# Performance work log

Measured on AMD Instinct MI355X. Metric: run time of the kernel, lower is better.

The kernel has to match this reference:

```python
import jax, jax.numpy as jnp
import numpy as np

B, L, D_MODEL = 8, 1024, 512
D_STATE, D_CONV, EXPAND = 16, 4, 2
D_INNER = EXPAND * D_MODEL          # 1024
DT_RANK = (D_MODEL + 15) // 16      # 32
D_FF = 4 * D_MODEL                  # 2048
EPS = 1e-12


def setup_inputs() -> dict:
    key = jax.random.key(0)
    ks = jax.random.split(key, 16)
    s = 0.02
    n = lambda k, shp: jax.random.normal(k, shp, dtype=jnp.float32) * s
    A = jnp.tile(jnp.arange(1, D_STATE + 1, dtype=jnp.float32)[None, :], (D_INNER, 1))
    return {
        "x": jax.random.normal(ks[0], (B, L, D_MODEL), dtype=jnp.float32),
        "in_proj_w": n(ks[1], (2 * D_INNER, D_MODEL)),
        "conv_w": n(ks[2], (D_INNER, 1, D_CONV)),
        "conv_b": jnp.zeros((D_INNER,), jnp.float32),
        "x_proj_w": n(ks[3], (DT_RANK + 2 * D_STATE, D_INNER)),
        "dt_proj_w": n(ks[4], (D_INNER, DT_RANK)),
        "dt_proj_b": jnp.full((D_INNER,), -4.0, jnp.float32),  # softplus(~-4) -> small dt
        "A_log": jnp.log(A),
        "D": jnp.ones((D_INNER,), jnp.float32),
        "out_proj_w": n(ks[5], (D_MODEL, D_INNER)),
        "ln1_g": jnp.ones((D_MODEL,), jnp.float32),
        "ln1_b": jnp.zeros((D_MODEL,), jnp.float32),
        "fc1_w": n(ks[6], (D_FF, D_MODEL)),
        "fc1_b": jnp.zeros((D_FF,), jnp.float32),
        "fc2_w": n(ks[7], (D_MODEL, D_FF)),
        "fc2_b": jnp.zeros((D_MODEL,), jnp.float32),
        "ln2_g": jnp.ones((D_MODEL,), jnp.float32),
        "ln2_b": jnp.zeros((D_MODEL,), jnp.float32),
    }


def _layernorm(x, g, b):
    m = jnp.mean(x, axis=-1, keepdims=True)
    v = jnp.var(x, axis=-1, keepdims=True)
    return (x - m) * jax.lax.rsqrt(v + EPS) * g + b


def _mamba(x, in_proj_w, conv_w, conv_b, x_proj_w, dt_proj_w, dt_proj_b, A_log, D, out_proj_w):
    # in_proj: [B,L,d_model] -> [B,L,2*d_inner]
    xz = jnp.einsum("bld,ed->ble", x, in_proj_w)
    u, z = jnp.split(xz, 2, axis=-1)                      # each [B,L,d_inner]
    # depthwise causal conv over time
    uc = jax.lax.conv_general_dilated(
        jnp.transpose(u, (0, 2, 1)), conv_w,
        window_strides=(1,), padding=[(D_CONV - 1, 0)],
        feature_group_count=D_INNER,
        dimension_numbers=("NCH", "OIH", "NCH"))
    u = jnp.transpose(uc, (0, 2, 1)) + conv_b             # [B,L,d_inner]
    u = jax.nn.silu(u)
    # x_proj -> dt, B, C
    x_dbl = jnp.einsum("bld,ed->ble", u, x_proj_w)
    dt, Bm, Cm = jnp.split(x_dbl, [DT_RANK, DT_RANK + D_STATE], axis=-1)
    dt = jax.nn.softplus(jnp.einsum("blr,dr->bld", dt, dt_proj_w) + dt_proj_b)  # [B,L,d_inner]
    A = -jnp.exp(A_log)                                   # [d_inner, d_state]
    deltaA = jnp.exp(dt[..., None] * A)                   # [B,L,d_inner,d_state]
    deltaBu = dt[..., None] * Bm[:, :, None, :] * u[..., None]

    def step(h, inp):
        dA_t, dBu_t, C_t = inp                            # [B,di,ds],[B,di,ds],[B,ds]
        h = h * dA_t + dBu_t
        y = jnp.einsum("bds,bs->bd", h, C_t)
        return h, y

    h0 = jnp.zeros((x.shape[0], D_INNER, D_STATE), x.dtype)
    _, ys = jax.lax.scan(step, h0, (jnp.transpose(deltaA, (1, 0, 2, 3)),
                                    jnp.transpose(deltaBu, (1, 0, 2, 3)),
                                    jnp.transpose(Cm, (1, 0, 2))))
    y = jnp.transpose(ys, (1, 0, 2)) + u * D              # [B,L,d_inner]
    y = y * jax.nn.silu(z)
    return jnp.einsum("ble,de->bld", y, out_proj_w)


def reference(x, in_proj_w, conv_w, conv_b, x_proj_w, dt_proj_w, dt_proj_b, A_log, D,
              out_proj_w, ln1_g, ln1_b, fc1_w, fc1_b, fc2_w, fc2_b, ln2_g, ln2_b):
    h = _mamba(x, in_proj_w, conv_w, conv_b, x_proj_w, dt_proj_w, dt_proj_b,
               A_log, D, out_proj_w)
    h = _layernorm(h + x, ln1_g, ln1_b)                   # dropout = identity (eval)
    # FeedForward with residual + LayerNorm
    f = jax.nn.gelu(jnp.einsum("bld,fd->blf", h, fc1_w) + fc1_b, approximate=False)
    f = jnp.einsum("blf,df->bld", f, fc2_w) + fc2_b
    return _layernorm(f + h, ln2_g, ln2_b)
```

## Files before the change

kernel.cpp:

```cpp
#include <hip/hip_runtime.h>
#include <hip/hip_bf16.h>
#include <math.h>

typedef __hip_bfloat16 bf16;
typedef unsigned short u16;
typedef unsigned int u32;
typedef __attribute__((ext_vector_type(8))) short short8;
typedef __attribute__((ext_vector_type(4))) float f32x4;
typedef __attribute__((ext_vector_type(4))) u32 u32x4;

#define B_  8
#define L_  1024
#define DM  512
#define DI  1024
#define DS  16
#define DR  32
#define DF  2048
#define M_  (B_ * L_)

__device__ __forceinline__ float b2f(bf16 x) { return __bfloat162float(x); }
__device__ __forceinline__ bf16  f2b(float x) { return __float2bfloat16(x); }
__device__ __forceinline__ u16   bu(bf16 x)  { return __builtin_bit_cast(u16, x); }
__device__ __forceinline__ float s2f(short x) { return b2f(__builtin_bit_cast(bf16, (u16)x)); }
__device__ __forceinline__ float uphi(u32 w) { return __builtin_bit_cast(float, w & 0xffff0000u); }
__device__ __forceinline__ float uplo(u32 w) { return __builtin_bit_cast(float, w << 16); }

__device__ __forceinline__ bool is_b16(const void* flag) {
    return ((const u16*)flag)[0] == 0x3F80;
}
__device__ __forceinline__ float ldr(const void* p, size_t i, bool b16) {
    return b16 ? b2f(((const bf16*)p)[i]) : ((const float*)p)[i];
}

__device__ __forceinline__ float fexp2(float x) {
#if __has_builtin(__builtin_amdgcn_exp2f)
    return __builtin_amdgcn_exp2f(x);
#else
    return __expf(x * 0.6931471805599453f);
#endif
}

__device__ __forceinline__ float fsoftplus(float v) {
    return (v > 20.f) ? v : __logf(1.f + __expf(v));
}

__device__ __forceinline__ float fgelu(float v) {
    const float x = v * 0.7071067811865475f;
    const float ax = fabsf(x);
    const float t = __builtin_amdgcn_rcpf(fmaf(0.3275911f, ax, 1.f));
    float p = fmaf(1.061405429f, t, -1.453152027f);
    p = fmaf(p, t, 1.421413741f);
    p = fmaf(p, t, -0.284496736f);
    p = fmaf(p, t, 0.254829592f);
    const float e = __expf(-ax * ax);
    float erf = 1.f - p * t * e;
    erf = (x < 0.f) ? -erf : erf;
    return 0.5f * v * (1.f + erf);
}

__device__ __forceinline__ void gload16(const bf16* g, bf16* l) {
    __builtin_amdgcn_global_load_lds(
        (const __attribute__((address_space(1))) unsigned int*)g,
        (__attribute__((address_space(3))) unsigned int*)l, 16, 0, 0);
}

__device__ __forceinline__ float fsilu(float x) {
    return x * __builtin_amdgcn_rcpf(1.f + __expf(-x));
}

#define CN0 (M_ * DM)
#define CN1 (CN0 + 2 * DI * DM)
#define CN2 (CN1 + 64 * DI)
#define CN3 (CN2 + DI * DR)
#define CN4 (CN3 + DM * DI)
#define CN5 (CN4 + DF * DM)
#define CN6 (CN5 + DM * DF)
#define CN7 (CN6 + DI * 4)
#define CN8 (CN7 + DI)
#define CN9 (CN8 + DI)
__global__ __launch_bounds__(256) void cvt_all_kernel(
    const void* s0, const void* s1, const void* s2, const void* s3,
    const void* s4, const void* s5, const void* s6, const void* s7,
    const void* s8, const void* s9,
    bf16* __restrict__ dst, const void* __restrict__ flag)
{
    const bool b16 = is_b16(flag);
    const long i = ((long)blockIdx.x * 256 + threadIdx.x) * 8;
    if (i >= CN9) return;
    const void* src; long off;
    if      (i < CN0) { src = s0; off = i; }
    else if (i < CN1) { src = s1; off = i - CN0; }
    else if (i < CN2) { src = s2; off = i - CN1; }
    else if (i < CN3) { src = s3; off = i - CN2; }
    else if (i < CN4) { src = s4; off = i - CN3; }
    else if (i < CN5) { src = s5; off = i - CN4; }
    else if (i < CN6) { src = s6; off = i - CN5; }
    else if (i < CN7) { src = s7; off = i - CN6; }
    else if (i < CN8) { src = s8; off = i - CN7; }
    else              { src = s9; off = i - CN8; }
    if (b16) {
        *(short8*)(dst + i) = *(const short8*)((const bf16*)src + off);
    } else {
        const float* f = (const float*)src + off;
        const f32x4 a = *(const f32x4*)f;
        const f32x4 b = *(const f32x4*)(f + 4);
        short8 o;
#pragma unroll
        for (int k = 0; k < 4; ++k) {
            o[k]     = (short)bu(f2b(a[k]));
            o[k + 4] = (short)bu(f2b(b[k]));
        }
        *(short8*)(dst + i) = o;
    }
}

template <int BM, int BN, int NT, int ACT, int PACK>
__global__ __launch_bounds__(NT) void mfma_gemm(
    const bf16* __restrict__ A, int lda,
    const bf16* __restrict__ W, int ldw,
    const void* __restrict__ bias,
    bf16* __restrict__ C, int ldc,
    int K, const void* __restrict__ flag,
    void* __restrict__ pk, void* __restrict__ pk2,
    const bf16* __restrict__ uin)
{
    constexpr int WN = (BN >= 128) ? 2 : 1;
    constexpr int CA = BM * 4 / NT;
    constexpr int CB = BN * 4 / NT;
    constexpr int BUF = (BM + BN) * 32;
    __shared__ __align__(16) bf16 smem[2 * BUF];
    const int tid  = threadIdx.x;
    const int wave = tid >> 6, lane = tid & 63;
    const int quad = lane >> 4, l16 = lane & 15;
    const u32 gx  = gridDim.x;
    const u32 nwg = gx * gridDim.y;
    const u32 lid = blockIdx.y * gx + blockIdx.x;
    const u32 swz = (lid & 7) * (nwg >> 3) + (lid >> 3);
    const int bm = (int)(swz / gx) * BM, bn = (int)(swz % gx) * BN;
    const int wm = (wave / WN) * 64, wn = (wave % WN) * 64;

    f32x4 acc[4][4];
#pragma unroll
    for (int i = 0; i < 4; ++i)
#pragma unroll
        for (int j = 0; j < 4; ++j) acc[i][j] = (f32x4){0.f, 0.f, 0.f, 0.f};

    auto load_tile = [&](int k0, int p) {
        bf16* As = smem + p * BUF;
        bf16* Ws = As + BM * 32;
#pragma unroll
        for (int j = 0; j < CA; ++j) {
            const int e = j * NT + tid;
            gload16(A + (size_t)(bm + (e >> 2)) * lda + k0 + (e & 3) * 8, As + e * 8);
        }
#pragma unroll
        for (int j = 0; j < CB; ++j) {
            const int e = j * NT + tid;
            gload16(W + (size_t)(bn + (e >> 2)) * ldw + k0 + (e & 3) * 8, Ws + e * 8);
        }
    };

    const int NIT = K >> 5;
    load_tile(0, 0);
    for (int it = 0; it < NIT; ++it) {
        __syncthreads();
        if (it + 1 < NIT) load_tile((it + 1) << 5, (it + 1) & 1);
        const bf16* As = smem + (it & 1) * BUF;
        const bf16* Ws = As + BM * 32;
        short8 af[4], wf[4];
#pragma unroll
        for (int mt = 0; mt < 4; ++mt)
            af[mt] = *(const short8*)(As + (wm + mt * 16 + l16) * 32 + quad * 8);
#pragma unroll
        for (int nt = 0; nt < 4; ++nt)
            wf[nt] = *(const short8*)(Ws + (wn + nt * 16 + l16) * 32 + quad * 8);
#pragma unroll
        for (int mt = 0; mt < 4; ++mt)
#pragma unroll
            for (int nt = 0; nt < 4; ++nt)
                acc[mt][nt] = __builtin_amdgcn_mfma_f32_16x16x32_bf16(
                    af[mt], wf[nt], acc[mt][nt], 0, 0, 0);
    }

    const bool b16 = bias ? is_b16(flag) : false;
#pragma unroll
    for (int nt = 0; nt < 4; ++nt) {
        const int col = bn + wn + nt * 16 + l16;
        const float bv = bias ? ldr(bias, col, b16) : 0.f;
#pragma unroll
        for (int mt = 0; mt < 4; ++mt)
#pragma unroll
            for (int i = 0; i < 4; ++i) {
                const int row = bm + wm + mt * 16 + quad * 4 + i;
                float v = acc[mt][nt][i] + bv;
                if (ACT == 1) v = fsoftplus(v);
                else if (ACT == 2) v = fgelu(v);
                if (PACK == 1) {
                    const float uv = b2f(uin[(size_t)row * ldc + col]);
                    ((float*)pk)[(size_t)row * ldc + col]  = v;
                    ((float*)pk2)[(size_t)row * ldc + col] = v * uv;
                } else {
                    C[(size_t)row * ldc + col] = f2b(v);
                }
            }
    }
    if (PACK == 2) {
#pragma unroll
        for (int mt = 0; mt < 4; ++mt)
#pragma unroll
            for (int i = 0; i < 4; ++i) {
                const int row = bm + wm + mt * 16 + quad * 4 + i;
                ((float*)pk)[(size_t)row * 16 + l16]  = acc[mt][2][i];
                ((float*)pk2)[(size_t)row * 16 + l16] = acc[mt][3][i];
            }
    }
}

__global__ __launch_bounds__(256) void conv_silu_kernel(
    const bf16* __restrict__ xz,
    const bf16* __restrict__ cw,
    const bf16* __restrict__ cb,
    const bf16* __restrict__ Dw,
    bf16* __restrict__ u,
    u32* __restrict__ ug)
{
    const int t  = blockIdx.x * 256 + threadIdx.x;
    const long t8 = (long)t * 8;
    const int d8  = (int)(t8 & (DI - 1));
    const int row = (int)(t8 >> 10);
    const int l   = row & (L_ - 1);

    short8 wraw[4];
#pragma unroll
    for (int k = 0; k < 4; ++k)
        wraw[k] = *(const short8*)(cw + (size_t)d8 * 4 + k * 8);
    const short8 cbv = *(const short8*)(cb + d8);
    const short8 dv  = *(const short8*)(Dw + d8);

    float acc[8];
#pragma unroll
    for (int i = 0; i < 8; ++i) acc[i] = s2f(cbv[i]);
#pragma unroll
    for (int j = 0; j < 4; ++j) {
        const int ls = l - 3 + j;
        if (ls >= 0) {
            const short8 xv = *(const short8*)(xz + (size_t)(row - 3 + j) * (2 * DI) + d8);
#pragma unroll
            for (int i = 0; i < 8; ++i) {
                const int f = i * 4 + j;
                acc[i] += s2f(wraw[f >> 3][f & 7]) * s2f(xv[i]);
            }
        }
    }
    const short8 zv = *(const short8*)(xz + (size_t)row * (2 * DI) + DI + d8);
    short8 us;
    u32x4 g0, g1;
#pragma unroll
    for (int i = 0; i < 8; ++i) {
        const float uv = fsilu(acc[i]);
        us[i] = (short)bu(f2b(uv));
        const float gz = fsilu(s2f(zv[i]));
        const float g2 = uv * s2f(dv[i]) * gz;
        const u32 p = ((u32)bu(f2b(g2)) << 16) | bu(f2b(gz));
        if (i < 4) g0[i] = p; else g1[i - 4] = p;
    }
    *(short8*)(u + t8) = us;
    *(u32x4*)(ug + t8) = g0;
    *(u32x4*)(ug + t8 + 4) = g1;
}

__global__ __launch_bounds__(256) void scan_kernel(
    const float* __restrict__ dtf,
    const float* __restrict__ duf,
    const float* __restrict__ Bf,
    const float* __restrict__ Cf,
    const u32* __restrict__ ug,
    const void* __restrict__ A_log,
    bf16* __restrict__ y,
    const void* __restrict__ flag)
{
    const bool b16 = is_b16(flag);
    const int tid = threadIdx.x;
    const int lane = tid & 63;
    const int s  = lane & 15;
    const int dl = tid >> 4;
    const int b = blockIdx.x >> 6, dch = blockIdx.x & 63;
    const int d0 = dch * 16, d = d0 + dl;
    const float AcL = -__expf(ldr(A_log, (size_t)d * DS + s, b16))
                      * 1.4426950408889634f;

    __shared__ __align__(16) float dt_s[16][68];
    __shared__ __align__(16) float du_s[16][68];
    __shared__ __align__(16) float B_s[16][68];
    __shared__ __align__(16) float C_s[16][68];
    __shared__ u32 ug_s[16][68];
    __shared__ bf16 y_s[16][72];
    __shared__ float p_s[16][16][33];

    const int c16 = tid & 15, r16 = tid >> 4;
    float rdt[4], rdu[4], rB[4], rC[4];
    u32 rug[4];
    const size_t base = (size_t)b * L_;

    auto load_chunk = [&](int l0) {
#pragma unroll
        for (int j = 0; j < 4; ++j) {
            const size_t row = base + l0 + r16 + 16 * j;
            rdt[j] = dtf[row * DI + d0 + c16];
            rdu[j] = duf[row * DI + d0 + c16];
            rug[j] = ug[row * DI + d0 + c16];
            rB[j]  = Bf[row * 16 + c16];
            rC[j]  = Cf[row * 16 + c16];
        }
    };
    auto store_chunk = [&]() {
#pragma unroll
        for (int j = 0; j < 4; ++j) {
            dt_s[c16][r16 + 16 * j] = rdt[j];
            du_s[c16][r16 + 16 * j] = rdu[j];
            ug_s[c16][r16 + 16 * j] = rug[j];
            B_s[c16][r16 + 16 * j]  = rB[j];
            C_s[c16][r16 + 16 * j]  = rC[j];
        }
    };

    float h = 0.f;
    float* const prow = &p_s[dl][s][0];
    load_chunk(0);
    for (int c = 0; c < 16; ++c) {
        store_chunk();
        __syncthreads();
        if (c < 15) load_chunk((c + 1) * 64);
#pragma unroll
        for (int g = 0; g < 2; ++g) {
#pragma unroll
            for (int w2 = 0; w2 < 2; ++w2) {
                const int w = g * 2 + w2;
                f32x4 dtw[4], duw[4], bw[4], cw[4];
#pragma unroll
                for (int q = 0; q < 4; ++q) {
                    dtw[q] = *(const f32x4*)&dt_s[dl][w * 16 + q * 4];
                    duw[q] = *(const f32x4*)&du_s[dl][w * 16 + q * 4];
                    bw[q]  = *(const f32x4*)&B_s[s][w * 16 + q * 4];
                    cw[q]  = *(const f32x4*)&C_s[s][w * 16 + q * 4];
                }
#pragma unroll
                for (int t = 0; t < 16; ++t) {
                    const float e = fexp2(dtw[t >> 2][t & 3] * AcL);
                    h = fmaf(h, e, duw[t >> 2][t & 3] * bw[t >> 2][t & 3]);
                    prow[w2 * 16 + t] = h * cw[t >> 2][t & 3];
                }
            }
            asm volatile("s_waitcnt lgkmcnt(0)" ::: "memory");
#pragma unroll
            for (int w2 = 0; w2 < 2; ++w2) {
                const int w = g * 2 + w2;
                const u32 ugw = ug_s[dl][w * 16 + s];
                float pr[16];
#pragma unroll
                for (int k = 0; k < 16; ++k) pr[k] = p_s[dl][k][w2 * 16 + s];
#pragma unroll
                for (int o = 8; o >= 1; o >>= 1)
#pragma unroll
                    for (int i = 0; i < o; ++i) pr[i] += pr[i + o];
                y_s[dl][w * 16 + s] = f2b(fmaf(pr[0], uplo(ugw), uphi(ugw)));
            }
        }
        __syncthreads();
#pragma unroll
        for (int j = 0; j < 4; ++j) {
            const size_t row = base + c * 64 + r16 + 16 * j;
            y[row * DI + d0 + c16] = y_s[c16][r16 + 16 * j];
        }
    }
}

template <int RMODE, int OMODE>
__global__ __launch_bounds__(256) void ln_kernel(
    const bf16* __restrict__ inp,
    const bf16* __restrict__ res,
    const void* __restrict__ g,
    const void* __restrict__ bb,
    void* __restrict__ out,
    const void* __restrict__ flag)
{
    const bool b16 = is_b16(flag);
    const int wv = threadIdx.x >> 6, lane = threadIdx.x & 63;
    const int row = blockIdx.x * 4 + wv;
    const size_t off = (size_t)row * DM;
    const int e = lane * 8;

    float v[8];
    const short8 iv = *(const short8*)(inp + off + e);
    const short8 rv = *(const short8*)(res + off + e);
#pragma unroll
    for (int i = 0; i < 8; ++i) v[i] = s2f(iv[i]) + s2f(rv[i]);

    float sum = 0.f, sq = 0.f;
#pragma unroll
    for (int i = 0; i < 8; ++i) { sum += v[i]; sq += v[i] * v[i]; }
#pragma unroll
    for (int o = 32; o >= 1; o >>= 1) {
        sum += __shfl_xor(sum, o);
        sq  += __shfl_xor(sq, o);
    }
    const float m = sum * (1.f / DM);
    const float var = sq * (1.f / DM) - m * m;
    const float inv = rsqrtf(fmaxf(var, 0.f) + 1e-12f);

    float gv[8], bv[8];
    if (b16) {
        const short8 gg = *(const short8*)((const bf16*)g + e);
        const short8 bg = *(const short8*)((const bf16*)bb + e);
#pragma unroll
        for (int i = 0; i < 8; ++i) { gv[i] = s2f(gg[i]); bv[i] = s2f(bg[i]); }
    } else {
        const float* gf = (const float*)g + e;
        const float* bf = (const float*)bb + e;
        const f32x4 g0 = *(const f32x4*)gf, g1 = *(const f32x4*)(gf + 4);
        const f32x4 b0 = *(const f32x4*)bf, b1 = *(const f32x4*)(bf + 4);
#pragma unroll
        for (int i = 0; i < 8; ++i) {
            gv[i] = i < 4 ? g0[i] : g1[i - 4];
            bv[i] = i < 4 ? b0[i] : b1[i - 4];
        }
    }
    float o[8];
#pragma unroll
    for (int i = 0; i < 8; ++i) o[i] = (v[i] - m) * inv * gv[i] + bv[i];

    if (OMODE == 2 && !b16) {
        f32x4 o0, o1;
#pragma unroll
        for (int i = 0; i < 4; ++i) { o0[i] = o[i]; o1[i] = o[i + 4]; }
        *(f32x4*)((float*)out + off + e) = o0;
        *(f32x4*)((float*)out + off + e + 4) = o1;
    } else {
        short8 os;
#pragma unroll
        for (int i = 0; i < 8; ++i) os[i] = (short)bu(f2b(o[i]));
        *(short8*)((bf16*)out + off + e) = os;
    }
}

extern "C" void kernel_launch(void* const* d_in, const int* in_sizes, int n_in,
                              void* d_out, int out_size, void* d_ws, size_t ws_size,
                              hipStream_t stream)
{
    (void)in_sizes; (void)n_in; (void)out_size; (void)ws_size;
    const void* x       = d_in[0];
    const void* in_w    = d_in[1];
    const void* conv_w  = d_in[2];
    const void* conv_b  = d_in[3];
    const void* xproj_w = d_in[4];
    const void* dt_w    = d_in[5];
    const void* dt_b    = d_in[6];
    const void* A_log   = d_in[7];
    const void* Dw      = d_in[8];
    const void* out_w   = d_in[9];
    const void* ln1_g   = d_in[10];
    const void* ln1_b   = d_in[11];
    const void* fc1_w   = d_in[12];
    const void* fc1_b   = d_in[13];
    const void* fc2_w   = d_in[14];
    const void* fc2_b   = d_in[15];
    const void* ln2_g   = d_in[16];
    const void* ln2_b   = d_in[17];
    const void* flag    = ln1_g;

    bf16* xb    = (bf16*)d_ws;
    bf16* inwb  = xb    + (size_t)M_ * DM;
    bf16* xpwb  = inwb  + (size_t)2 * DI * DM;
    bf16* dtwb  = xpwb  + (size_t)64 * DI;
    bf16* outwb = dtwb  + (size_t)DI * DR;
    bf16* fc1wb = outwb + (size_t)DM * DI;
    bf16* fc2wb = fc1wb + (size_t)DF * DM;
    bf16* cwb   = fc2wb + (size_t)DM * DF;
    bf16* cbb   = cwb   + (size_t)DI * 4;
    bf16* dwb   = cbb   + (size_t)DI;
    bf16* xz    = dwb   + (size_t)DI;
    bf16* u     = xz    + (size_t)M_ * 2 * DI;
    bf16* xdbl  = u     + (size_t)M_ * DI;
    float* dtf  = (float*)(xdbl + (size_t)M_ * 64);
    u32*  ugp   = (u32*)(dtf + (size_t)M_ * DI);
    float* Bfp  = (float*)(ugp + (size_t)M_ * DI);
    bf16* yb    = (bf16*)(Bfp + (size_t)M_ * 16);
    bf16* hb    = yb    + (size_t)M_ * DI;
    float* duf  = (float*)xz;
    float* Cfp  = (float*)hb;
    bf16* mo    = (bf16*)dtf;
    bf16* fb    = xz;
    bf16* f2b_  = yb;

    dim3 blk(256);
    cvt_all_kernel<<<dim3((CN9 / 8 + 255) / 256), blk, 0, stream>>>(
        x, in_w, xproj_w, dt_w, out_w, fc1_w, fc2_w, conv_w, conv_b, Dw,
        xb, flag);

    mfma_gemm<128, 128, 256, 0, 0><<<dim3(16, 64), blk, 0, stream>>>(
        xb, DM, inwb, DM, nullptr, xz, 2 * DI, DM, flag, nullptr, nullptr, nullptr);
    conv_silu_kernel<<<dim3(M_ * DI / 8 / 256), blk, 0, stream>>>(
        xz, cwb, cbb, dwb, u, ugp);
    mfma_gemm<128, 64, 128, 0, 2><<<dim3(1, 64), dim3(128), 0, stream>>>(
        u, DI, xpwb, DI, nullptr, xdbl, 64, DI, flag, Bfp, Cfp, nullptr);
    mfma_gemm<128, 128, 256, 1, 1><<<dim3(8, 64), blk, 0, stream>>>(
        xdbl, 64, dtwb, DR, dt_b, nullptr, DI, DR, flag, dtf, duf, u);
    scan_kernel<<<dim3(B_ * 64), blk, 0, stream>>>(
        dtf, duf, Bfp, Cfp, ugp, A_log, yb, flag);
    mfma_gemm<128, 128, 256, 0, 0><<<dim3(4, 64), blk, 0, stream>>>(
        yb, DI, outwb, DI, nullptr, mo, DM, DI, flag, nullptr, nullptr, nullptr);
    ln_kernel<1, 1><<<dim3(M_ / 4), blk, 0, stream>>>(
        mo, xb, ln1_g, ln1_b, hb, flag);
    mfma_gemm<128, 128, 256, 2, 0><<<dim3(16, 64), blk, 0, stream>>>(
        hb, DM, fc1wb, DM, fc1_b, fb, DF, DM, flag, nullptr, nullptr, nullptr);
    mfma_gemm<128, 128, 256, 0, 0><<<dim3(4, 64), blk, 0, stream>>>(
        fb, DF, fc2wb, DF, fc2_b, f2b_, DM, DF, flag, nullptr, nullptr, nullptr);
    ln_kernel<1, 2><<<dim3(M_ / 4), blk, 0, stream>>>(
        f2b_, hb, ln2_g, ln2_b, d_out, flag);
}
```

Measured before the change: 344.4 us.

## Fuse dt_proj GEMM and softplus into scan kernel via per-chunk MFMA

```diff
diff --git a/kernel.cpp b/kernel.cpp
--- a/kernel.cpp
+++ b/kernel.cpp
@@ -195,13 +195,7 @@
                 float v = acc[mt][nt][i] + bv;
                 if (ACT == 1) v = fsoftplus(v);
                 else if (ACT == 2) v = fgelu(v);
-                if (PACK == 1) {
-                    const float uv = b2f(uin[(size_t)row * ldc + col]);
-                    ((float*)pk)[(size_t)row * ldc + col]  = v;
-                    ((float*)pk2)[(size_t)row * ldc + col] = v * uv;
-                } else {
-                    C[(size_t)row * ldc + col] = f2b(v);
-                }
+                C[(size_t)row * ldc + col] = f2b(v);
             }
     }
     if (PACK == 2) {
@@ -270,12 +264,14 @@
 }
 
 __global__ __launch_bounds__(256) void scan_kernel(
-    const float* __restrict__ dtf,
-    const float* __restrict__ duf,
+    const bf16* __restrict__ xdbl,
+    const bf16* __restrict__ u,
     const float* __restrict__ Bf,
     const float* __restrict__ Cf,
     const u32* __restrict__ ug,
     const void* __restrict__ A_log,
+    const bf16* __restrict__ dtw,
+    const void* __restrict__ dt_b,
     bf16* __restrict__ y,
     const void* __restrict__ flag)
 {
@@ -284,10 +280,15 @@
     const int lane = tid & 63;
     const int s  = lane & 15;
     const int dl = tid >> 4;
+    const int quad = dl & 3;
+    const int v = tid >> 6;
     const int b = blockIdx.x >> 6, dch = blockIdx.x & 63;
     const int d0 = dch * 16, d = d0 + dl;
     const float AcL = -__expf(ldr(A_log, (size_t)d * DS + s, b16))
                       * 1.4426950408889634f;
+
+    const short8 wfrag = *(const short8*)(dtw + (size_t)(d0 + s) * DR + quad * 8);
+    const float dtb = ldr(dt_b, d0 + s, b16);
 
     __shared__ __align__(16) float dt_s[16][68];
     __shared__ __align__(16) float du_s[16][68];
@@ -298,30 +299,45 @@
     __shared__ float p_s[16][16][33];
 
     const int c16 = tid & 15, r16 = tid >> 4;
-    float rdt[4], rdu[4], rB[4], rC[4];
+    float rB[4], rC[4];
     u32 rug[4];
+    short8 rxd;
+    u16 ru4[4];
     const size_t base = (size_t)b * L_;
 
     auto load_chunk = [&](int l0) {
 #pragma unroll
         for (int j = 0; j < 4; ++j) {
             const size_t row = base + l0 + r16 + 16 * j;
-            rdt[j] = dtf[row * DI + d0 + c16];
-            rdu[j] = duf[row * DI + d0 + c16];
             rug[j] = ug[row * DI + d0 + c16];
             rB[j]  = Bf[row * 16 + c16];
             rC[j]  = Cf[row * 16 + c16];
         }
+        rxd = *(const short8*)(xdbl + (size_t)(base + l0 + v * 16 + s) * 64
+                               + quad * 8);
+#pragma unroll
+        for (int i = 0; i < 4; ++i)
+            ru4[i] = ((const u16*)u)[(size_t)(base + l0 + v * 16 + quad * 4 + i)
+                                     * DI + d0 + s];
     };
     auto store_chunk = [&]() {
 #pragma unroll
         for (int j = 0; j < 4; ++j) {
-            dt_s[c16][r16 + 16 * j] = rdt[j];
-            du_s[c16][r16 + 16 * j] = rdu[j];
             ug_s[c16][r16 + 16 * j] = rug[j];
             B_s[c16][r16 + 16 * j]  = rB[j];
             C_s[c16][r16 + 16 * j]  = rC[j];
         }
+        f32x4 a0 = __builtin_amdgcn_mfma_f32_16x16x32_bf16(
+            rxd, wfrag, (f32x4){0.f, 0.f, 0.f, 0.f}, 0, 0, 0);
+        f32x4 dtv, duv;
+#pragma unroll
+        for (int i = 0; i < 4; ++i) {
+            const float t = fsoftplus(a0[i] + dtb);
+            dtv[i] = t;
+            duv[i] = t * s2f((short)ru4[i]);
+        }
+        *(f32x4*)&dt_s[s][v * 16 + quad * 4] = dtv;
+        *(f32x4*)&du_s[s][v * 16 + quad * 4] = duv;
     };
 
     float h = 0.f;
@@ -336,17 +352,17 @@
 #pragma unroll
             for (int w2 = 0; w2 < 2; ++w2) {
                 const int w = g * 2 + w2;
-                f32x4 dtw[4], duw[4], bw[4], cw[4];
+                f32x4 dtw4[4], duw[4], bw[4], cw[4];
 #pragma unroll
                 for (int q = 0; q < 4; ++q) {
-                    dtw[q] = *(const f32x4*)&dt_s[dl][w * 16 + q * 4];
-                    duw[q] = *(const f32x4*)&du_s[dl][w * 16 + q * 4];
-                    bw[q]  = *(const f32x4*)&B_s[s][w * 16 + q * 4];
-                    cw[q]  = *(const f32x4*)&C_s[s][w * 16 + q * 4];
+                    dtw4[q] = *(const f32x4*)&dt_s[dl][w * 16 + q * 4];
+                    duw[q]  = *(const f32x4*)&du_s[dl][w * 16 + q * 4];
+                    bw[q]   = *(const f32x4*)&B_s[s][w * 16 + q * 4];
+                    cw[q]   = *(const f32x4*)&C_s[s][w * 16 + q * 4];
                 }
 #pragma unroll
                 for (int t = 0; t < 16; ++t) {
-                    const float e = fexp2(dtw[t >> 2][t & 3] * AcL);
+                    const float e = fexp2(dtw4[t >> 2][t & 3] * AcL);
                     h = fmaf(h, e, duw[t >> 2][t & 3] * bw[t >> 2][t & 3]);
                     prow[w2 * 16 + t] = h * cw[t >> 2][t & 3];
                 }
@@ -486,7 +502,6 @@
     float* Bfp  = (float*)(ugp + (size_t)M_ * DI);
     bf16* yb    = (bf16*)(Bfp + (size_t)M_ * 16);
     bf16* hb    = yb    + (size_t)M_ * DI;
-    float* duf  = (float*)xz;
     float* Cfp  = (float*)hb;
     bf16* mo    = (bf16*)dtf;
     bf16* fb    = xz;
@@ -503,10 +518,8 @@
         xz, cwb, cbb, dwb, u, ugp);
     mfma_gemm<128, 64, 128, 0, 2><<<dim3(1, 64), dim3(128), 0, stream>>>(
         u, DI, xpwb, DI, nullptr, xdbl, 64, DI, flag, Bfp, Cfp, nullptr);
-    mfma_gemm<128, 128, 256, 1, 1><<<dim3(8, 64), blk, 0, stream>>>(
-        xdbl, 64, dtwb, DR, dt_b, nullptr, DI, DR, flag, dtf, duf, u);
     scan_kernel<<<dim3(B_ * 64), blk, 0, stream>>>(
-        dtf, duf, Bfp, Cfp, ugp, A_log, yb, flag);
+        xdbl, u, Bfp, Cfp, ugp, A_log, dtwb, dt_b, yb, flag);
     mfma_gemm<128, 128, 256, 0, 0><<<dim3(4, 64), blk, 0, stream>>>(
         yb, DI, outwb, DI, nullptr, mo, DM, DI, flag, nullptr, nullptr, nullptr);
     ln_kernel<1, 1><<<dim3(M_ / 4), blk, 0, stream>>>(
```

Result: faster. 326.8 us (-5.1%).
